# Kernel optimization log

Measured on AMD Instinct MI355X. Metric: run time of the kernel, lower is better.

Reference implementation:

```python
import jax, jax.numpy as jnp
import numpy as np

C = 256
B, H, W = 16, 48, 48


def setup_inputs() -> dict:
    key = jax.random.key(0)
    ks = jax.random.split(key, 9)
    s = 1.0 / np.sqrt(C)
    return {
        "x": jax.random.normal(ks[0], (B, C, H, W), dtype=jnp.float32),
        "Wq": jax.random.normal(ks[1], (C, C), dtype=jnp.float32) * s,
        "bq": jax.random.normal(ks[2], (C,), dtype=jnp.float32) * s,
        "Wk": jax.random.normal(ks[3], (C, C), dtype=jnp.float32) * s,
        "bk": jax.random.normal(ks[4], (C,), dtype=jnp.float32) * s,
        "Wv": jax.random.normal(ks[5], (C, C), dtype=jnp.float32) * s,
        "bv": jax.random.normal(ks[6], (C,), dtype=jnp.float32) * s,
        "rel_h": jax.random.normal(ks[7], (1, C, 1, H), dtype=jnp.float32),
        "rel_w": jax.random.normal(ks[8], (1, C, W, 1), dtype=jnp.float32),
    }


def reference(x, Wq, bq, Wk, bk, Wv, bv, rel_h, rel_w):
    b, c, h, w = x.shape
    n = h * w
    # 1x1 conv == per-pixel linear over channels
    def proj(Wp, bp):
        y = jnp.einsum('bchw,oc->bohw', x, Wp) + bp[None, :, None, None]
        return y.reshape(b, c, n)
    q = proj(Wq, bq)  # [B, C, N]
    k = proj(Wk, bk)
    v = proj(Wv, bv)
    # content-content: q^T k -> [B, N, N]
    cc = jnp.einsum('bcn,bcm->bnm', q, k)
    # relative position term: (rel_h + rel_w) -> [1, C, W, H] -> [C, N]
    pos = (rel_h + rel_w).reshape(c, n)
    # content-position: pos^T @ q -> [B, N, N]
    cp = jnp.einsum('cn,bcm->bnm', pos, q)
    att = jax.nn.softmax(cc + cp, axis=-1)  # [B, N, N]
    # out[b,c,n] = sum_m v[b,c,m] * att[b,n,m]
    out = jnp.einsum('bcm,bnm->bcn', v, att)
    return out.reshape(b, c, h, w)
```

## Files before the change

kernel.cpp:

```cpp
#include <hip/hip_runtime.h>
#include <hip/hip_bf16.h>


#define BB 16
#define CC 256
#define HH 48
#define NN 2304

typedef float f32x4 __attribute__((ext_vector_type(4)));
typedef short bf16x8 __attribute__((ext_vector_type(8)));
typedef _Float16 f16x8 __attribute__((ext_vector_type(8)));

#define MFMA(a, b, c)  __builtin_amdgcn_mfma_f32_16x16x32_bf16((a), (b), (c), 0, 0, 0)
#define MFMAH(a, b, c) __builtin_amdgcn_mfma_f32_16x16x32_f16((a), (b), (c), 0, 0, 0)

__device__ inline bf16x8 ldg8(const __hip_bfloat16* p) {
    return *reinterpret_cast<const bf16x8*>(p);
}
__device__ inline f16x8 ldh8(const _Float16* p) {
    return *reinterpret_cast<const f16x8*>(p);
}
__device__ inline float bf2f(unsigned short v) {
    unsigned u = (unsigned)v << 16;
    float f;
    __builtin_memcpy(&f, &u, 4);
    return f;
}

typedef __attribute__((address_space(3))) unsigned int lds_uint;
typedef const __attribute__((address_space(1))) unsigned int gbl_uint;

__device__ inline void gload_lds16(const void* g, void* l) {
    __builtin_amdgcn_global_load_lds((gbl_uint*)g, (lds_uint*)l, 16, 0, 0);
}

__global__ __launch_bounds__(256) void k_prep_w(const float* __restrict__ Wq,
        const float* __restrict__ Wk, const float* __restrict__ Wv,
        _Float16* __restrict__ w) {
    int i = blockIdx.x * 256 + threadIdx.x;
    int m = i >> 16, j = i & 65535;
    const float* W = (m == 0) ? Wq : ((m == 1) ? Wk : Wv);
    w[i] = (_Float16)W[j];
}

__global__ __launch_bounds__(256) void k_prep_rel(const float* __restrict__ rel_h,
        const float* __restrict__ rel_w,
        _Float16* __restrict__ relhT, _Float16* __restrict__ relwT) {
    int i = blockIdx.x * 256 + threadIdx.x;
    int h = i >> 8, c = i & 255;
    relhT[i] = (_Float16)rel_h[c * HH + h];
    relwT[i] = (_Float16)rel_w[c * HH + h];
}

__global__ __launch_bounds__(256) void k_projqkv(
        const float* __restrict__ x,
        const _Float16* __restrict__ w,
        const float* __restrict__ bq, const float* __restrict__ bk, const float* __restrict__ bv,
        _Float16* __restrict__ qt_hi, _Float16* __restrict__ qt_lo,
        _Float16* __restrict__ kt,
        __hip_bfloat16* __restrict__ vbuf) {
    __shared__ float xf[32][257];
    __shared__ __align__(16) _Float16 lds_a[2][32][256];
    int b = blockIdx.y;
    int n0 = blockIdx.x * 32;
    int t = threadIdx.x;
    int wave = t >> 6, lane = t & 63;
    int lr = lane & 15, lg = lane >> 4;
    int o0 = wave * 64;
    const size_t bN = (size_t)b * NN;

    {
        int nj = t & 31, cg = t >> 5;
        #pragma unroll
        for (int it = 0; it < 32; ++it) {
            int c = it * 8 + cg;
            xf[nj][c] = x[((size_t)b * CC + c) * NN + n0 + nj];
        }
    }
    __syncthreads();
    {
        int r = t & 31, cg = t >> 5;
        #pragma unroll
        for (int i = 0; i < 32; ++i) {
            int c = cg + 8 * i;
            float v = xf[r][c];
            _Float16 h = (_Float16)v;
            int pc = (((c >> 3) ^ (r & 7)) << 3) | (c & 7);
            lds_a[0][r][pc] = h;
            lds_a[1][r][pc] = (_Float16)(v - (float)h);
        }
    }
    __syncthreads();

    #pragma unroll
    for (int pj = 0; pj < 3; ++pj) {
        const _Float16* wp = w + (size_t)pj * 65536;
        f32x4 acc[2][4] = {};
        #pragma unroll
        for (int ks = 0; ks < 8; ++ks) {
            int kk = ks * 32 + lg * 8;
            f16x8 ah[2], al[2];
            #pragma unroll
            for (int nt = 0; nt < 2; ++nt) {
                int row = nt * 16 + lr;
                int ch = ((ks * 4 + lg) ^ (lr & 7)) * 8;
                ah[nt] = *reinterpret_cast<const f16x8*>(&lds_a[0][row][ch]);
                al[nt] = *reinterpret_cast<const f16x8*>(&lds_a[1][row][ch]);
            }
            #pragma unroll
            for (int ot = 0; ot < 4; ++ot) {
                int rowB = o0 + ot * 16 + lr;
                f16x8 bh = ldh8(wp + rowB * CC + kk);
                #pragma unroll
                for (int nt = 0; nt < 2; ++nt) {
                    acc[nt][ot] = MFMAH(ah[nt], bh, acc[nt][ot]);
                    if (pj < 2) acc[nt][ot] = MFMAH(al[nt], bh, acc[nt][ot]);
                }
            }
        }
        const float* bias = (pj == 0) ? bq : ((pj == 1) ? bk : bv);
        #pragma unroll
        for (int ot = 0; ot < 4; ++ot) {
            int o = o0 + ot * 16 + lr;
            float bb = bias[o];
            #pragma unroll
            for (int nt = 0; nt < 2; ++nt) {
                #pragma unroll
                for (int r = 0; r < 4; ++r) {
                    int n = n0 + nt * 16 + lg * 4 + r;
                    float y = acc[nt][ot][r] + bb;
                    if (pj == 0) {
                        _Float16 h = (_Float16)y;
                        size_t off = (bN + n) * CC + o;
                        qt_hi[off] = h;
                        qt_lo[off] = (_Float16)(y - (float)h);
                    } else if (pj == 1) {
                        kt[(bN + n) * CC + o] = (_Float16)y;
                    } else {
                        vbuf[((size_t)b * CC + o) * NN + n] = __float2bfloat16(y);
                    }
                }
            }
        }
    }
}

__global__ __launch_bounds__(256) void k_posq(
        const _Float16* __restrict__ qt_hi, const _Float16* __restrict__ qt_lo,
        const _Float16* __restrict__ relhT, const _Float16* __restrict__ relwT,
        float* __restrict__ rhq, float* __restrict__ rwq) {
    int b = blockIdx.y, m0 = blockIdx.x * 64;
    int wave = threadIdx.x >> 6, lane = threadIdx.x & 63;
    int lr = lane & 15, lg = lane >> 4;
    int m = m0 + wave * 16 + lr;
    const size_t bN = (size_t)b * NN;
    f32x4 acc[6] = {};
    #pragma unroll
    for (int ks = 0; ks < 8; ++ks) {
        int kk = ks * 32 + lg * 8;
        f16x8 bhf = ldh8(qt_hi + (bN + m) * CC + kk);
        f16x8 blf = ldh8(qt_lo + (bN + m) * CC + kk);
        #pragma unroll
        for (int t = 0; t < 3; ++t) {
            int rowH = t * 16 + lr;
            f16x8 ahh = ldh8(relhT + rowH * CC + kk);
            acc[t] = MFMAH(ahh, bhf, acc[t]);
            acc[t] = MFMAH(ahh, blf, acc[t]);
            f16x8 awh = ldh8(relwT + rowH * CC + kk);
            acc[3 + t] = MFMAH(awh, bhf, acc[3 + t]);
            acc[3 + t] = MFMAH(awh, blf, acc[3 + t]);
        }
    }
    #pragma unroll
    for (int t = 0; t < 3; ++t) {
        #pragma unroll
        for (int r = 0; r < 4; ++r) {
            int h = t * 16 + lg * 4 + r;
            rhq[((size_t)b * HH + h) * NN + m] = acc[t][r];
            rwq[((size_t)b * HH + h) * NN + m] = acc[3 + t][r];
        }
    }
}

__global__ __launch_bounds__(512, 2) void k_attn(
        const _Float16* __restrict__ qt_hi,
        const _Float16* __restrict__ kt,
        const float* __restrict__ rhq, const float* __restrict__ rwq,
        const __hip_bfloat16* __restrict__ vbuf,
        __hip_bfloat16* __restrict__ o0, __hip_bfloat16* __restrict__ o1,
        __hip_bfloat16* __restrict__ o2, __hip_bfloat16* __restrict__ o3,
        float2* __restrict__ ml, int tpb) {
    __shared__ __align__(16) _Float16 lds_k[2][64][128];
    __shared__ __align__(16) __hip_bfloat16 lds_v[256][64];
    __shared__ __align__(16) __hip_bfloat16 lds_p[128][64];
    float* lds_scale = reinterpret_cast<float*>(&lds_k[1][0][0]);
    int*   lds_flag  = reinterpret_cast<int*>(lds_scale + 128);
    int b = blockIdx.y;
    int n0 = blockIdx.x * 128;
    int z = blockIdx.z;
    int t0 = z * tpb, t_end = t0 + tpb;
    __hip_bfloat16* opart = (z == 0) ? o0 : (z == 1) ? o1 : (z == 2) ? o2 : o3;
    int wave = threadIdx.x >> 6, lane = threadIdx.x & 63;
    int lr = lane & 15, lg = lane >> 4;
    int rowA = n0 + wave * 16 + lr;
    const size_t bN = (size_t)b * NN;

    f16x8 qh[8];
    #pragma unroll
    for (int ks = 0; ks < 8; ++ks) {
        int kk = ks * 32 + lg * 8;
        qh[ks] = ldh8(qt_hi + (bN + rowA) * CC + kk);
    }
    int hn[4], wn[4];
    #pragma unroll
    for (int r = 0; r < 4; ++r) {
        int n = n0 + wave * 16 + lg * 4 + r;
        hn[r] = n % HH;
        wn[r] = n / HH;
    }
    const float* rhq_b = rhq + (size_t)b * HH * NN;
    const float* rwq_b = rwq + (size_t)b * HH * NN;

    int nh = wave >> 2;
    int cq = wave & 3;
    f32x4 oacc[4][4] = {};
    float mrun[4] = {-1e30f, -1e30f, -1e30f, -1e30f};
    float lrun[4] = {0.f, 0.f, 0.f, 0.f};

    int krin = lane >> 4, kch = lane & 15;
    auto STAGE_K = [&](int buf, int m0s, int k0) {
        #pragma unroll
        for (int j = 0; j < 2; ++j) {
            int lrow = wave * 8 + j * 4;
            int grow = lrow + krin;
            gload_lds16(kt + (bN + m0s + grow) * CC + k0 + ((kch ^ (grow & 7)) * 8),
                        &lds_k[buf][lrow][0]);
        }
    };
    int srl = lane >> 3;
    int sch = ((lane & 7) ^ srl) * 8;
    auto STAGE_V = [&](int half, int m0s) {
        #pragma unroll
        for (int j = 0; j < 2; ++j) {
            int lrow = half * 128 + wave * 16 + j * 8;
            int crow = lrow + srl;
            gload_lds16(vbuf + ((size_t)b * CC + crow) * NN + m0s + sch, &lds_v[lrow][0]);
        }
    };

    STAGE_K(0, t0 * 64, 0);
    __syncthreads();

    for (int t = t0; t < t_end; ++t) {
        int m0 = t * 64;
        float padd[4][4];
        #pragma unroll
        for (int mt = 0; mt < 4; ++mt) {
            int m = m0 + mt * 16 + lr;
            #pragma unroll
            for (int r = 0; r < 4; ++r)
                padd[mt][r] = rhq_b[(size_t)hn[r] * NN + m] + rwq_b[(size_t)wn[r] * NN + m];
        }
        f32x4 sacc[4] = {};
        #pragma unroll
        for (int s = 0; s < 2; ++s) {
            if (s == 0) {
                STAGE_K(1, m0, 128);
                STAGE_V(0, m0);
            } else {
                int mn = (t + 1 < t_end) ? (t + 1) * 64 : t0 * 64;
                STAGE_K(0, mn, 0);
                STAGE_V(1, m0);
            }
            #pragma unroll
            for (int ks = 0; ks < 4; ++ks) {
                #pragma unroll
                for (int mt = 0; mt < 4; ++mt) {
                    int row = mt * 16 + lr;
                    int ch = ((ks * 4 + lg) ^ (lr & 7)) * 8;
                    f16x8 bh = *reinterpret_cast<const f16x8*>(&lds_k[s][row][ch]);
                    sacc[mt] = MFMAH(qh[s * 4 + ks], bh, sacc[mt]);
                }
            }
            __syncthreads();
        }
        #pragma unroll
        for (int mt = 0; mt < 4; ++mt)
            #pragma unroll
            for (int r = 0; r < 4; ++r)
                sacc[mt][r] += padd[mt][r];
        bool lane_need = false;
        #pragma unroll
        for (int mt = 0; mt < 4; ++mt)
            #pragma unroll
            for (int r = 0; r < 4; ++r)
                lane_need |= (sacc[mt][r] > mrun[r] + 8.0f);
        bool wave_need = __any(lane_need);
        float scl_r[4] = {1.f, 1.f, 1.f, 1.f};
        if (wave_need) {
            #pragma unroll
            for (int r = 0; r < 4; ++r) {
                float smax = fmaxf(fmaxf(sacc[0][r], sacc[1][r]),
                                   fmaxf(sacc[2][r], sacc[3][r]));
                #pragma unroll
                for (int mk = 1; mk <= 8; mk <<= 1)
                    smax = fmaxf(smax, __shfl_xor(smax, mk));
                float mnew = fmaxf(mrun[r], smax);
                scl_r[r] = __expf(mrun[r] - mnew);
                mrun[r] = mnew;
                lrun[r] *= scl_r[r];
            }
        }
        #pragma unroll
        for (int r = 0; r < 4; ++r) {
            float rsum = 0.f;
            #pragma unroll
            for (int mt = 0; mt < 4; ++mt) {
                float p = __expf(sacc[mt][r] - mrun[r]);
                sacc[mt][r] = p;
                rsum += p;
            }
            lrun[r] += rsum;
        }
        #pragma unroll
        for (int mt = 0; mt < 4; ++mt) {
            #pragma unroll
            for (int r = 0; r < 4; ++r) {
                int prow = wave * 16 + lg * 4 + r;
                int pcol = mt * 16 + lr;
                int pcol_s = (((pcol >> 3) ^ (prow & 7)) << 3) | (pcol & 7);
                lds_p[prow][pcol_s] = __float2bfloat16(sacc[mt][r]);
            }
        }
        if (lr == 0) {
            #pragma unroll
            for (int r = 0; r < 4; ++r)
                lds_scale[wave * 16 + lg * 4 + r] = scl_r[r];
        }
        if (lane == 0) lds_flag[wave] = wave_need ? 1 : 0;
        __syncthreads();
        int4 f0 = *reinterpret_cast<const int4*>(&lds_flag[0]);
        int4 f1 = *reinterpret_cast<const int4*>(&lds_flag[4]);
        bool do_scale = (f0.x | f0.y | f0.z | f0.w | f1.x | f1.y | f1.z | f1.w) != 0;
        if (do_scale) {
            #pragma unroll
            for (int nf = 0; nf < 4; ++nf) {
                f32x4 s4 = *reinterpret_cast<const f32x4*>(&lds_scale[nh * 64 + nf * 16 + lg * 4]);
                #pragma unroll
                for (int cf = 0; cf < 4; ++cf)
                    oacc[nf][cf] *= s4;
            }
        }
        #pragma unroll
        for (int ks2 = 0; ks2 < 2; ++ks2) {
            bf16x8 pa[4];
            #pragma unroll
            for (int nf = 0; nf < 4; ++nf) {
                int prow = nh * 64 + nf * 16 + lr;
                int pch = ((ks2 * 4 + lg) ^ (lr & 7)) * 8;
                pa[nf] = *reinterpret_cast<const bf16x8*>(&lds_p[prow][pch]);
            }
            #pragma unroll
            for (int cf = 0; cf < 4; ++cf) {
                int vrow = cq * 64 + cf * 16 + lr;
                int vch = ((ks2 * 4 + lg) ^ (lr & 7)) * 8;
                bf16x8 bv = *reinterpret_cast<const bf16x8*>(&lds_v[vrow][vch]);
                #pragma unroll
                for (int nf = 0; nf < 4; ++nf)
                    oacc[nf][cf] = MFMA(pa[nf], bv, oacc[nf][cf]);
            }
        }
        __syncthreads();
    }
    #pragma unroll
    for (int r = 0; r < 4; ++r) {
        #pragma unroll
        for (int mk = 1; mk <= 8; mk <<= 1)
            lrun[r] += __shfl_xor(lrun[r], mk);
    }
    if (lr == 0) {
        #pragma unroll
        for (int r = 0; r < 4; ++r) {
            int n = n0 + wave * 16 + lg * 4 + r;
            ml[((size_t)z * BB + b) * NN + n] = make_float2(mrun[r], lrun[r]);
        }
    }
    #pragma unroll
    for (int nf = 0; nf < 4; ++nf) {
        int nbase = n0 + nh * 64 + nf * 16 + lg * 4;
        #pragma unroll
        for (int cf = 0; cf < 4; ++cf) {
            int c = cq * 64 + cf * 16 + lr;
            union { ushort4 u4; unsigned short us[4]; } pk;
            #pragma unroll
            for (int j = 0; j < 4; ++j) {
                __hip_bfloat16 hv = __float2bfloat16(oacc[nf][cf][j]);
                pk.us[j] = *reinterpret_cast<unsigned short*>(&hv);
            }
            *reinterpret_cast<ushort4*>(&opart[((size_t)b * CC + c) * NN + nbase]) = pk.u4;
        }
    }
}

__global__ __launch_bounds__(256) void k_combine(
        const __hip_bfloat16* __restrict__ o0, const __hip_bfloat16* __restrict__ o1,
        const __hip_bfloat16* __restrict__ o2, const __hip_bfloat16* __restrict__ o3,
        const float2* __restrict__ ml, int nsplit, float* __restrict__ out) {
    size_t idx = ((size_t)blockIdx.x * 256 + threadIdx.x) * 4;
    int n4 = (int)(idx % NN);
    int c  = (int)((idx / NN) % CC);
    int b  = (int)(idx / ((size_t)NN * CC));
    float M[4] = {-1e30f, -1e30f, -1e30f, -1e30f};
    for (int zz = 0; zz < nsplit; ++zz) {
        #pragma unroll
        for (int j = 0; j < 4; ++j)
            M[j] = fmaxf(M[j], ml[((size_t)zz * BB + b) * NN + n4 + j].x);
    }
    float num[4] = {}, den[4] = {};
    for (int zz = 0; zz < nsplit; ++zz) {
        const __hip_bfloat16* op = (zz == 0) ? o0 : (zz == 1) ? o1 : (zz == 2) ? o2 : o3;
        ushort4 u = *reinterpret_cast<const ushort4*>(op + ((size_t)b * CC + c) * NN + n4);
        unsigned short us[4] = {u.x, u.y, u.z, u.w};
        #pragma unroll
        for (int j = 0; j < 4; ++j) {
            float2 v = ml[((size_t)zz * BB + b) * NN + n4 + j];
            float w = __expf(v.x - M[j]);
            num[j] += bf2f(us[j]) * w;
            den[j] += v.y * w;
        }
    }
    f32x4 o;
    #pragma unroll
    for (int j = 0; j < 4; ++j) o[j] = num[j] / den[j];
    *reinterpret_cast<f32x4*>(&out[idx]) = o;
}

extern "C" void kernel_launch(void* const* d_in, const int* in_sizes, int n_in,
                              void* d_out, int out_size, void* d_ws, size_t ws_size,
                              hipStream_t stream) {
    const float* x     = (const float*)d_in[0];
    const float* Wq    = (const float*)d_in[1];
    const float* bq    = (const float*)d_in[2];
    const float* Wk    = (const float*)d_in[3];
    const float* bk    = (const float*)d_in[4];
    const float* Wv    = (const float*)d_in[5];
    const float* bv    = (const float*)d_in[6];
    const float* rel_h = (const float*)d_in[7];
    const float* rel_w = (const float*)d_in[8];
    float* out = (float*)d_out;

    size_t off = 0;
    auto carve = [&](size_t bytes) {
        void* p = (char*)d_ws + off;
        off += (bytes + 255) & ~(size_t)255;
        return p;
    };
    const size_t sz_t = (size_t)BB * NN * CC * 2;
    _Float16* qt_hi  = (_Float16*)carve(sz_t);
    _Float16* qt_lo  = (_Float16*)carve(sz_t);
    _Float16* kt     = (_Float16*)carve(sz_t);
    __hip_bfloat16* vbuf = (__hip_bfloat16*)carve(sz_t);
    _Float16* relhT = (_Float16*)carve((size_t)HH * CC * 2);
    _Float16* relwT = (_Float16*)carve((size_t)HH * CC * 2);
    _Float16* w     = (_Float16*)carve((size_t)3 * CC * CC * 2);
    float* rhq = (float*)carve((size_t)BB * HH * NN * 4);
    float* rwq = (float*)carve((size_t)BB * HH * NN * 4);
    float2* ml = (float2*)carve((size_t)4 * BB * NN * sizeof(float2));
    __hip_bfloat16* o0 = (__hip_bfloat16*)carve(sz_t);
    __hip_bfloat16* o1 = (__hip_bfloat16*)carve(sz_t);
    if (off > ws_size) return;

    __hip_bfloat16* o2 = nullptr;
    __hip_bfloat16* o3 = nullptr;
    int nsplit = 2;
    {
        size_t save = off;
        __hip_bfloat16* p2 = (__hip_bfloat16*)carve(sz_t);
        __hip_bfloat16* p3 = (__hip_bfloat16*)carve(sz_t);
        if (off <= ws_size) { nsplit = 4; o2 = p2; o3 = p3; }
        else { off = save; }
    }
    int tpb = 36 / nsplit;

    k_prep_w<<<dim3(3 * CC * CC / 256), 256, 0, stream>>>(Wq, Wk, Wv, w);
    k_prep_rel<<<dim3(HH * CC / 256), 256, 0, stream>>>(rel_h, rel_w, relhT, relwT);
    k_projqkv<<<dim3(NN / 32, BB), 256, 0, stream>>>(
        x, w, bq, bk, bv, qt_hi, qt_lo, kt, vbuf);
    k_posq<<<dim3(NN / 64, BB), 256, 0, stream>>>(
        qt_hi, qt_lo, relhT, relwT, rhq, rwq);
    k_attn<<<dim3(NN / 128, BB, nsplit), 512, 0, stream>>>(
        qt_hi, kt, rhq, rwq, vbuf, o0, o1, o2, o3, ml, tpb);
    k_combine<<<dim3((size_t)BB * CC * NN / 1024), 256, 0, stream>>>(
        o0, o1, o2, o3, ml, nsplit, out);
}
```

Before: 444.8 us.

## Fuse positional q projection into QKV kernel and stage V stores through LDS

Computes the rel_h/rel_w dot products with q inside the projection kernel, reading the q tile from shared memory instead of writing q_lo to global and launching a separate posq kernel. This removes the q_lo buffer, one launch, and the global round trip of q. V output is transposed through LDS so it can be written to global as coalesced 16-byte vectors. The trade-off is more per-block work and extra barriers in the projection kernel, plus reuse of the xf shared buffer for staging.

```diff
diff --git a/kernel.cpp b/kernel.cpp
--- a/kernel.cpp
+++ b/kernel.cpp
@@ -56,11 +56,14 @@
         const float* __restrict__ x,
         const _Float16* __restrict__ w,
         const float* __restrict__ bq, const float* __restrict__ bk, const float* __restrict__ bv,
-        _Float16* __restrict__ qt_hi, _Float16* __restrict__ qt_lo,
-        _Float16* __restrict__ kt,
-        __hip_bfloat16* __restrict__ vbuf) {
+        const _Float16* __restrict__ relhT, const _Float16* __restrict__ relwT,
+        _Float16* __restrict__ qt_hi, _Float16* __restrict__ kt,
+        __hip_bfloat16* __restrict__ vbuf,
+        float* __restrict__ rhq, float* __restrict__ rwq) {
     __shared__ float xf[32][257];
     __shared__ __align__(16) _Float16 lds_a[2][32][256];
+    _Float16* qlds = reinterpret_cast<_Float16*>(&xf[0][0]);
+    __hip_bfloat16* vt = reinterpret_cast<__hip_bfloat16*>(&xf[0][0]);
     int b = blockIdx.y;
     int n0 = blockIdx.x * 32;
     int t = threadIdx.x;
@@ -92,9 +95,8 @@
     }
     __syncthreads();
 
-    #pragma unroll
-    for (int pj = 0; pj < 3; ++pj) {
-        const _Float16* wp = w + (size_t)pj * 65536;
+    {
+        const _Float16* wp = w;
         f32x4 acc[2][4] = {};
         #pragma unroll
         for (int ks = 0; ks < 8; ++ks) {
@@ -114,70 +116,143 @@
                 #pragma unroll
                 for (int nt = 0; nt < 2; ++nt) {
                     acc[nt][ot] = MFMAH(ah[nt], bh, acc[nt][ot]);
-                    if (pj < 2) acc[nt][ot] = MFMAH(al[nt], bh, acc[nt][ot]);
+                    acc[nt][ot] = MFMAH(al[nt], bh, acc[nt][ot]);
                 }
             }
         }
-        const float* bias = (pj == 0) ? bq : ((pj == 1) ? bk : bv);
         #pragma unroll
         for (int ot = 0; ot < 4; ++ot) {
             int o = o0 + ot * 16 + lr;
-            float bb = bias[o];
+            float bb = bq[o];
             #pragma unroll
             for (int nt = 0; nt < 2; ++nt) {
                 #pragma unroll
                 for (int r = 0; r < 4; ++r) {
-                    int n = n0 + nt * 16 + lg * 4 + r;
+                    int nl = nt * 16 + lg * 4 + r;
                     float y = acc[nt][ot][r] + bb;
-                    if (pj == 0) {
-                        _Float16 h = (_Float16)y;
-                        size_t off = (bN + n) * CC + o;
-                        qt_hi[off] = h;
-                        qt_lo[off] = (_Float16)(y - (float)h);
-                    } else if (pj == 1) {
-                        kt[(bN + n) * CC + o] = (_Float16)y;
-                    } else {
-                        vbuf[((size_t)b * CC + o) * NN + n] = __float2bfloat16(y);
-                    }
+                    _Float16 h = (_Float16)y;
+                    _Float16 lo = (_Float16)(y - (float)h);
+                    qt_hi[(bN + n0 + nl) * CC + o] = h;
+                    int pc = (((o >> 3) ^ (nl & 7)) << 3) | (o & 7);
+                    qlds[nl * 256 + pc] = h;
+                    qlds[8192 + nl * 256 + pc] = lo;
                 }
             }
         }
     }
-}
-
-__global__ __launch_bounds__(256) void k_posq(
-        const _Float16* __restrict__ qt_hi, const _Float16* __restrict__ qt_lo,
-        const _Float16* __restrict__ relhT, const _Float16* __restrict__ relwT,
-        float* __restrict__ rhq, float* __restrict__ rwq) {
-    int b = blockIdx.y, m0 = blockIdx.x * 64;
-    int wave = threadIdx.x >> 6, lane = threadIdx.x & 63;
-    int lr = lane & 15, lg = lane >> 4;
-    int m = m0 + wave * 16 + lr;
-    const size_t bN = (size_t)b * NN;
-    f32x4 acc[6] = {};
-    #pragma unroll
-    for (int ks = 0; ks < 8; ++ks) {
-        int kk = ks * 32 + lg * 8;
-        f16x8 bhf = ldh8(qt_hi + (bN + m) * CC + kk);
-        f16x8 blf = ldh8(qt_lo + (bN + m) * CC + kk);
-        #pragma unroll
-        for (int t = 0; t < 3; ++t) {
-            int rowH = t * 16 + lr;
-            f16x8 ahh = ldh8(relhT + rowH * CC + kk);
-            acc[t] = MFMAH(ahh, bhf, acc[t]);
-            acc[t] = MFMAH(ahh, blf, acc[t]);
-            f16x8 awh = ldh8(relwT + rowH * CC + kk);
-            acc[3 + t] = MFMAH(awh, bhf, acc[3 + t]);
-            acc[3 + t] = MFMAH(awh, blf, acc[3 + t]);
-        }
-    }
-    #pragma unroll
-    for (int t = 0; t < 3; ++t) {
-        #pragma unroll
-        for (int r = 0; r < 4; ++r) {
-            int h = t * 16 + lg * 4 + r;
-            rhq[((size_t)b * HH + h) * NN + m] = acc[t][r];
-            rwq[((size_t)b * HH + h) * NN + m] = acc[3 + t][r];
+    __syncthreads();
+
+    {
+        int rel_sel = wave >> 1, mtile = wave & 1;
+        const _Float16* rel = rel_sel ? relwT : relhT;
+        float* rout = rel_sel ? rwq : rhq;
+        int brow = mtile * 16 + lr;
+        f32x4 pacc[3] = {};
+        #pragma unroll
+        for (int ks = 0; ks < 8; ++ks) {
+            int kk = ks * 32 + lg * 8;
+            int bch = ((ks * 4 + lg) ^ (brow & 7)) * 8;
+            f16x8 bh = *reinterpret_cast<const f16x8*>(&qlds[brow * 256 + bch]);
+            f16x8 bl = *reinterpret_cast<const f16x8*>(&qlds[8192 + brow * 256 + bch]);
+            #pragma unroll
+            for (int ht = 0; ht < 3; ++ht) {
+                f16x8 a = ldh8(rel + (ht * 16 + lr) * CC + kk);
+                pacc[ht] = MFMAH(a, bh, pacc[ht]);
+                pacc[ht] = MFMAH(a, bl, pacc[ht]);
+            }
+        }
+        #pragma unroll
+        for (int ht = 0; ht < 3; ++ht) {
+            #pragma unroll
+            for (int r = 0; r < 4; ++r) {
+                int h = ht * 16 + lg * 4 + r;
+                int m = n0 + mtile * 16 + lr;
+                rout[((size_t)b * HH + h) * NN + m] = pacc[ht][r];
+            }
+        }
+    }
+
+    {
+        const _Float16* wp = w + 65536;
+        f32x4 acc[2][4] = {};
+        #pragma unroll
+        for (int ks = 0; ks < 8; ++ks) {
+            int kk = ks * 32 + lg * 8;
+            f16x8 ah[2], al[2];
+            #pragma unroll
+            for (int nt = 0; nt < 2; ++nt) {
+                int row = nt * 16 + lr;
+                int ch = ((ks * 4 + lg) ^ (lr & 7)) * 8;
+                ah[nt] = *reinterpret_cast<const f16x8*>(&lds_a[0][row][ch]);
+                al[nt] = *reinterpret_cast<const f16x8*>(&lds_a[1][row][ch]);
+            }
+            #pragma unroll
+            for (int ot = 0; ot < 4; ++ot) {
+                int rowB = o0 + ot * 16 + lr;
+                f16x8 bh = ldh8(wp + rowB * CC + kk);
+                #pragma unroll
+                for (int nt = 0; nt < 2; ++nt) {
+                    acc[nt][ot] = MFMAH(ah[nt], bh, acc[nt][ot]);
+                    acc[nt][ot] = MFMAH(al[nt], bh, acc[nt][ot]);
+                }
+            }
+        }
+        #pragma unroll
+        for (int ot = 0; ot < 4; ++ot) {
+            int o = o0 + ot * 16 + lr;
+            float bb = bk[o];
+            #pragma unroll
+            for (int nt = 0; nt < 2; ++nt) {
+                #pragma unroll
+                for (int r = 0; r < 4; ++r) {
+                    int nl = nt * 16 + lg * 4 + r;
+                    kt[(bN + n0 + nl) * CC + o] = (_Float16)(acc[nt][ot][r] + bb);
+                }
+            }
+        }
+    }
+
+    {
+        const _Float16* wp = w + 2 * 65536;
+        f32x4 acc[2][4] = {};
+        #pragma unroll
+        for (int ks = 0; ks < 8; ++ks) {
+            int kk = ks * 32 + lg * 8;
+            f16x8 ah[2];
+            #pragma unroll
+            for (int nt = 0; nt < 2; ++nt) {
+                int row = nt * 16 + lr;
+                int ch = ((ks * 4 + lg) ^ (lr & 7)) * 8;
+                ah[nt] = *reinterpret_cast<const f16x8*>(&lds_a[0][row][ch]);
+            }
+            #pragma unroll
+            for (int ot = 0; ot < 4; ++ot) {
+                int rowB = o0 + ot * 16 + lr;
+                f16x8 bh = ldh8(wp + rowB * CC + kk);
+                #pragma unroll
+                for (int nt = 0; nt < 2; ++nt)
+                    acc[nt][ot] = MFMAH(ah[nt], bh, acc[nt][ot]);
+            }
+        }
+        __syncthreads();
+        #pragma unroll
+        for (int ot = 0; ot < 4; ++ot) {
+            int o = o0 + ot * 16 + lr;
+            float bb = bv[o];
+            #pragma unroll
+            for (int nt = 0; nt < 2; ++nt) {
+                #pragma unroll
+                for (int r = 0; r < 4; ++r) {
+                    int nl = nt * 16 + lg * 4 + r;
+                    vt[o * 40 + nl] = __float2bfloat16(acc[nt][ot][r] + bb);
+                }
+            }
+        }
+        __syncthreads();
+        #pragma unroll
+        for (int j = 0; j < 4; ++j) {
+            bf16x8 vv = *reinterpret_cast<const bf16x8*>(&vt[t * 40 + j * 8]);
+            *reinterpret_cast<bf16x8*>(&vbuf[((size_t)b * CC + t) * NN + n0 + j * 8]) = vv;
         }
     }
 }
@@ -457,7 +532,6 @@
     };
     const size_t sz_t = (size_t)BB * NN * CC * 2;
     _Float16* qt_hi  = (_Float16*)carve(sz_t);
-    _Float16* qt_lo  = (_Float16*)carve(sz_t);
     _Float16* kt     = (_Float16*)carve(sz_t);
     __hip_bfloat16* vbuf = (__hip_bfloat16*)carve(sz_t);
     _Float16* relhT = (_Float16*)carve((size_t)HH * CC * 2);
@@ -485,9 +559,7 @@
     k_prep_w<<<dim3(3 * CC * CC / 256), 256, 0, stream>>>(Wq, Wk, Wv, w);
     k_prep_rel<<<dim3(HH * CC / 256), 256, 0, stream>>>(rel_h, rel_w, relhT, relwT);
     k_projqkv<<<dim3(NN / 32, BB), 256, 0, stream>>>(
-        x, w, bq, bk, bv, qt_hi, qt_lo, kt, vbuf);
-    k_posq<<<dim3(NN / 64, BB), 256, 0, stream>>>(
-        qt_hi, qt_lo, relhT, relwT, rhq, rwq);
+        x, w, bq, bk, bv, relhT, relwT, qt_hi, kt, vbuf, rhq, rwq);
     k_attn<<<dim3(NN / 128, BB, nsplit), 512, 0, stream>>>(
         qt_hi, kt, rhq, rwq, vbuf, o0, o1, o2, o3, ml, tpb);
     k_combine<<<dim3((size_t)BB * CC * NN / 1024), 256, 0, stream>>>(
```

Result: faster. 404.4 us (median of 2 runs) (-9.1%).
